# Kernel tuning notes

Measured on AMD Instinct MI355X. Metric: run time of the kernel, lower is better.

Reference implementation:

```python
import jax, jax.numpy as jnp
import numpy as np

VIEWS = 32   # hardcoded in forward
K = 5        # LocalGCN k
D = 1024     # (34-2)*(34-2) flattened conv features per view
EPS = 1e-5   # BatchNorm eps


def leaky_relu(x, slope=0.2):
    return jnp.where(x >= 0, x, slope * x)


def setup_inputs() -> dict:
    key = jax.random.key(0)
    ks = jax.random.split(key, 8)
    B_img = 512 * VIEWS
    x = jax.random.normal(ks[0], (B_img, 3, 34, 34), jnp.float32)
    vertices = jax.random.normal(ks[1], (VIEWS, 3), jnp.float32)
    # Conv2d(3, 1, 3)
    conv_w = jax.random.normal(ks[2], (1, 3, 3, 3), jnp.float32) * 0.1
    conv_b = jnp.zeros((1,), jnp.float32)
    # relation MLP R: Linear(10,10) -> ReLU -> Linear(10,1)
    r_w1 = jax.random.normal(ks[3], (10, 10), jnp.float32) * 0.3
    r_b1 = jnp.zeros((10,), jnp.float32)
    r_w2 = jax.random.normal(ks[4], (1, 10), jnp.float32) * 0.3
    r_b2 = jnp.zeros((1,), jnp.float32)
    # LocalGCN conv: Linear(D, D) + BatchNorm1d(D)
    lin_w = jax.random.normal(ks[5], (D, D), jnp.float32) / np.sqrt(D)
    lin_b = jnp.zeros((D,), jnp.float32)
    bn_g = jnp.ones((D,), jnp.float32)
    bn_b = jnp.zeros((D,), jnp.float32)
    return dict(x=x, vertices=vertices, conv_w=conv_w, conv_b=conv_b,
                r_w1=r_w1, r_b1=r_b1, r_w2=r_w2, r_b2=r_b2,
                lin_w=lin_w, lin_b=lin_b, bn_g=bn_g, bn_b=bn_b)


def reference(x, vertices, conv_w, conv_b, r_w1, r_b1, r_w2, r_b2,
              lin_w, lin_b, bn_g, bn_b):
    # Conv2d(3->1, kernel 3, valid) : (B*32,3,34,34) -> (B*32,1,32,32)
    y = jax.lax.conv_general_dilated(
        x, conv_w, window_strides=(1, 1), padding='VALID',
        dimension_numbers=('NCHW', 'OIHW', 'NCHW'))
    y = y + conv_b[None, :, None, None]

    B = x.shape[0] // VIEWS
    F = y.reshape(B, VIEWS, D)                       # (B, N, D)
    V = jnp.broadcast_to(vertices[None], (B, VIEWS, 3))  # (B, N, 3)

    # knn over vertices: negative squared pairwise distance, topk largest
    inner = -2.0 * jnp.einsum('bnd,bmd->bnm', V, V)
    xx = jnp.sum(V * V, axis=-1, keepdims=True)
    pdist = -xx - inner - jnp.swapaxes(xx, 1, 2)     # (B, N, N)
    idx = jax.lax.top_k(pdist, K)[1]                 # (B, N, K)

    # index_points gathers
    Fn = jax.vmap(lambda p, i: p[i])(F, idx)         # (B, N, K, D)
    Vn = jax.vmap(lambda p, i: p[i])(V, idx)         # (B, N, K, 3)

    v0 = jnp.broadcast_to(Vn[:, :, :1, :], Vn.shape)
    dv = v0 - Vn
    dnorm = jnp.sqrt(jnp.sum(dv * dv, axis=-1, keepdims=True) + 1e-12)
    v_F = jnp.concatenate([v0, Vn, dv, dnorm], axis=-1)   # (B, N, K, 10)

    h = jax.nn.relu(v_F @ r_w1.T + r_b1)
    e = h @ r_w2.T + r_b2                            # (B, N, K, 1)

    Fa = jnp.sum(e * Fn, axis=2)                     # (B, N, D)

    flat = Fa.reshape(-1, D)
    z = flat @ lin_w.T + lin_b
    mean = jnp.mean(z, axis=0)
    var = jnp.var(z, axis=0)
    z = (z - mean) / jnp.sqrt(var + EPS) * bn_g + bn_b
    out = leaky_relu(z).reshape(-1, 1, D)            # n_views = 1
    return out
```

## Files before the change

kernel.cpp:

```cpp
#include <hip/hip_runtime.h>
#include <stdint.h>

typedef unsigned short u16;
using bf16x8 = __attribute__((ext_vector_type(8))) short;
using f32x4  = __attribute__((ext_vector_type(4))) float;

__device__ __forceinline__ float bf2f(u16 u) {
  union { unsigned int i; float f; } a; a.i = ((unsigned int)u) << 16; return a.f;
}
__device__ __forceinline__ u16 f2bf(float f) {
  union { float f; unsigned int i; } a; a.f = f;
  unsigned int u = a.i;
  u += 0x7fffu + ((u >> 16) & 1u);
  return (u16)(u >> 16);
}
__device__ __forceinline__ float lrelu(float x) { return x >= 0.f ? x : 0.2f * x; }

__global__ __launch_bounds__(256) void prep_convw_kernel(
    const float* __restrict__ vert, const float* __restrict__ rw1,
    const float* __restrict__ rb1, const float* __restrict__ rw2,
    const float* __restrict__ rb2, const float* __restrict__ lw,
    u16* __restrict__ wb, float* __restrict__ e_out,
    int* __restrict__ idx_out, float* __restrict__ stats) {
  const int t = threadIdx.x;
  if (blockIdx.x < 1024) {
    const int i = blockIdx.x * 256 + t;
    float4 v = ((const float4*)lw)[i];
    uint2 o;
    o.x = (unsigned)f2bf(v.x) | ((unsigned)f2bf(v.y) << 16);
    o.y = (unsigned)f2bf(v.z) | ((unsigned)f2bf(v.w) << 16);
    ((uint2*)wb)[i] = o;
    return;
  }
  __shared__ float Vs[96];
  __shared__ float w1s[100];
  __shared__ float b1s[10];
  __shared__ float w2s[10];
  __shared__ float b2s;
  if (t < 96)  Vs[t]  = vert[t];
  if (t < 100) w1s[t] = rw1[t];
  if (t < 10)  { b1s[t] = rb1[t]; w2s[t] = rw2[t]; }
  if (t == 0)  b2s = rb2[0];
  for (int i = t; i < 2048; i += 256) stats[i] = 0.f;
  __syncthreads();
  if (t < 32) {
    const float vt0 = Vs[t*3], vt1 = Vs[t*3+1], vt2 = Vs[t*3+2];
    const float xxt = vt0*vt0 + vt1*vt1 + vt2*vt2;
    float pd[32];
    #pragma unroll
    for (int m = 0; m < 32; ++m) {
      float m0 = Vs[m*3], m1 = Vs[m*3+1], m2 = Vs[m*3+2];
      float dot = vt0*m0 + vt1*m1 + vt2*m2;
      float inner = -2.f * dot;
      float xxm = m0*m0 + m1*m1 + m2*m2;
      pd[m] = -xxt - inner - xxm;
    }
    int sel[5];
    unsigned taken = 0;
    #pragma unroll
    for (int k = 0; k < 5; ++k) {
      float best = -3.0e38f; int bi = 0;
      #pragma unroll
      for (int m = 0; m < 32; ++m)
        if (!((taken >> m) & 1u) && pd[m] > best) { best = pd[m]; bi = m; }
      taken |= (1u << bi);
      sel[k] = bi;
    }
    const int s0 = sel[0];
    const float v0x = Vs[s0*3], v0y = Vs[s0*3+1], v0z = Vs[s0*3+2];
    #pragma unroll
    for (int k = 0; k < 5; ++k) {
      const int si = sel[k];
      float vx = Vs[si*3], vy = Vs[si*3+1], vz = Vs[si*3+2];
      float dx = v0x - vx, dy = v0y - vy, dz = v0z - vz;
      float dn = sqrtf(dx*dx + dy*dy + dz*dz + 1e-12f);
      float vF[10] = {v0x, v0y, v0z, vx, vy, vz, dx, dy, dz, dn};
      float e = b2s;
      #pragma unroll
      for (int i = 0; i < 10; ++i) {
        float h = b1s[i];
        #pragma unroll
        for (int j = 0; j < 10; ++j) h += w1s[i*10+j] * vF[j];
        h = h > 0.f ? h : 0.f;
        e += w2s[i] * h;
      }
      e_out[t*5+k]   = e;
      idx_out[t*5+k] = sel[k];
    }
  }
}

__global__ __launch_bounds__(256) void conv_kernel(const float* __restrict__ x,
    const float* __restrict__ cw, const float* __restrict__ cb, u16* __restrict__ F) {
  __shared__ __align__(16) float lds[3*34*34];
  const int t = threadIdx.x;
  const long img = blockIdx.x;
  const float4* src = (const float4*)(x + img * 3468);
  for (int q = t; q < 867; q += 256)
    ((float4*)lds)[q] = src[q];
  float w[27];
  #pragma unroll
  for (int q = 0; q < 27; ++q) w[q] = cw[q];
  const float bias = cb[0];
  __syncthreads();
  const int p0 = t * 4;
  const int i = p0 >> 5, j = p0 & 31;
  u16 r[4];
  #pragma unroll
  for (int u = 0; u < 4; ++u) {
    float acc = bias;
    #pragma unroll
    for (int c = 0; c < 3; ++c)
      #pragma unroll
      for (int dy = 0; dy < 3; ++dy)
        #pragma unroll
        for (int dxk = 0; dxk < 3; ++dxk)
          acc += w[c*9 + dy*3 + dxk] * lds[c*1156 + (i+dy)*34 + (j+u+dxk)];
    r[u] = f2bf(acc);
  }
  uint2 o;
  o.x = (unsigned)r[0] | ((unsigned)r[1] << 16);
  o.y = (unsigned)r[2] | ((unsigned)r[3] << 16);
  ((uint2*)(F + img*1024))[t] = o;
}

__global__ __launch_bounds__(256) void gather_kernel(const u16* __restrict__ F,
    const float* __restrict__ e, const int* __restrict__ idx, u16* __restrict__ Fa) {
  const int g = blockIdx.x;
  const int b = g >> 5, n = g & 31;
  const int t = threadIdx.x;
  float a0=0.f, a1=0.f, a2=0.f, a3=0.f;
  #pragma unroll
  for (int k = 0; k < 5; ++k) {
    const float ek = e[n*5+k];
    const int id = idx[n*5+k];
    uint2 d = ((const uint2*)(F + ((long)(b*32 + id)) * 1024))[t];
    a0 += ek * __uint_as_float(d.x << 16);
    a1 += ek * __uint_as_float(d.x & 0xffff0000u);
    a2 += ek * __uint_as_float(d.y << 16);
    a3 += ek * __uint_as_float(d.y & 0xffff0000u);
  }
  uint2 o;
  o.x = (unsigned)f2bf(a0) | ((unsigned)f2bf(a1) << 16);
  o.y = (unsigned)f2bf(a2) | ((unsigned)f2bf(a3) << 16);
  ((uint2*)(Fa + (long)g * 1024))[t] = o;
}

__global__ __launch_bounds__(256) void gemm_kernel(const u16* __restrict__ A,
    const u16* __restrict__ W, const float* __restrict__ linb, u16* __restrict__ z,
    float* __restrict__ stats) {
  __shared__ __align__(16) u16 At[128*32];
  __shared__ __align__(16) u16 Bt[128*32];
  const int t = threadIdx.x;
  const int lane = t & 63;
  const int w = t >> 6;
  const int lr = lane & 15, lq = lane >> 4;
  const int wm = w >> 1, wn = w & 1;
  const long m0 = (long)blockIdx.y * 128;
  const int n0 = blockIdx.x * 128;
  f32x4 acc[4][4];
  #pragma unroll
  for (int mi = 0; mi < 4; ++mi)
    #pragma unroll
    for (int ni = 0; ni < 4; ++ni) acc[mi][ni] = (f32x4){0.f, 0.f, 0.f, 0.f};
  const int srow = t >> 2;
  const int scol = (t & 3) * 8;
  for (int k0 = 0; k0 < 1024; k0 += 32) {
    #pragma unroll
    for (int h = 0; h < 2; ++h) {
      const u16* ga = A + (m0 + h*64 + srow) * 1024 + k0 + scol;
      const u16* gb = W + (long)(n0 + h*64 + srow) * 1024 + k0 + scol;
      __builtin_amdgcn_global_load_lds(
          (const __attribute__((address_space(1))) void*)ga,
          (__attribute__((address_space(3))) void*)((char*)At + h*4096 + t*16), 16, 0, 0);
      __builtin_amdgcn_global_load_lds(
          (const __attribute__((address_space(1))) void*)gb,
          (__attribute__((address_space(3))) void*)((char*)Bt + h*4096 + t*16), 16, 0, 0);
    }
    __syncthreads();
    bf16x8 af[4], bfr[4];
    #pragma unroll
    for (int i = 0; i < 4; ++i)
      af[i] = *(const bf16x8*)&At[(wm*64 + i*16 + lr)*32 + lq*8];
    #pragma unroll
    for (int i = 0; i < 4; ++i)
      bfr[i] = *(const bf16x8*)&Bt[(wn*64 + i*16 + lr)*32 + lq*8];
    #pragma unroll
    for (int mi = 0; mi < 4; ++mi)
      #pragma unroll
      for (int ni = 0; ni < 4; ++ni)
        acc[mi][ni] = __builtin_amdgcn_mfma_f32_16x16x32_bf16(af[mi], bfr[ni], acc[mi][ni], 0, 0, 0);
    __syncthreads();
  }
  #pragma unroll
  for (int ni = 0; ni < 4; ++ni) {
    const int col = n0 + wn*64 + ni*16 + lr;
    const float bias = linb[col];
    float s = 0.f, q = 0.f;
    #pragma unroll
    for (int mi = 0; mi < 4; ++mi) {
      const long row = m0 + wm*64 + mi*16 + lq*4;
      #pragma unroll
      for (int r = 0; r < 4; ++r) {
        const float v = acc[mi][ni][r] + bias;
        z[(row + r) * 1024 + col] = f2bf(v);
        s += v; q += v * v;
      }
    }
    s += __shfl_xor(s, 16); q += __shfl_xor(q, 16);
    s += __shfl_xor(s, 32); q += __shfl_xor(q, 32);
    if (lq == 0) {
      atomicAdd(&stats[col], s);
      atomicAdd(&stats[1024 + col], q);
    }
  }
}

__global__ void finalize_kernel(float* __restrict__ stats, const float* __restrict__ g,
                                const float* __restrict__ b, int Mrows) {
  const float invM = 1.f / (float)Mrows;
  for (int c = threadIdx.x; c < 1024; c += 256) {
    float mean = stats[c] * invM;
    float var  = stats[1024+c] * invM - mean*mean;
    float rstd = rsqrtf(var + 1e-5f);
    float sc = g[c] * rstd;
    float sh = b[c] - mean * sc;
    stats[c] = sc;
    stats[1024+c] = sh;
  }
}

__global__ __launch_bounds__(256) void norm_kernel(const u16* __restrict__ z,
    const float* __restrict__ stats, float* __restrict__ out) {
  const long i = (long)blockIdx.x * 256 + threadIdx.x;
  uint2 d = ((const uint2*)z)[i];
  const int c = ((int)(i * 4)) & 1023;
  float v0 = __uint_as_float(d.x << 16);
  float v1 = __uint_as_float(d.x & 0xffff0000u);
  float v2 = __uint_as_float(d.y << 16);
  float v3 = __uint_as_float(d.y & 0xffff0000u);
  float4 y;
  y.x = lrelu(v0 * stats[c+0] + stats[1024+c+0]);
  y.y = lrelu(v1 * stats[c+1] + stats[1024+c+1]);
  y.z = lrelu(v2 * stats[c+2] + stats[1024+c+2]);
  y.w = lrelu(v3 * stats[c+3] + stats[1024+c+3]);
  ((float4*)out)[i] = y;
}

extern "C" void kernel_launch(void* const* d_in, const int* in_sizes, int n_in,
                              void* d_out, int out_size, void* d_ws, size_t ws_size,
                              hipStream_t stream) {
  const float* x    = (const float*)d_in[0];
  const float* vert = (const float*)d_in[1];
  const float* cw   = (const float*)d_in[2];
  const float* cb   = (const float*)d_in[3];
  const float* rw1  = (const float*)d_in[4];
  const float* rb1  = (const float*)d_in[5];
  const float* rw2  = (const float*)d_in[6];
  const float* rb2  = (const float*)d_in[7];
  const float* lw   = (const float*)d_in[8];
  const float* lb   = (const float*)d_in[9];
  const float* bng  = (const float*)d_in[10];
  const float* bnb  = (const float*)d_in[11];
  float* out = (float*)d_out;

  const int n_img = in_sizes[0] / (3*34*34);
  const size_t faBytes = (size_t)n_img * 1024 * 2;

  char* ws = (char*)d_ws;
  u16*  Fa = (u16*)ws;
  u16*  F  = (u16*)(ws + faBytes);
  u16*  z  = (u16*)(ws + faBytes);
  char* sp = ws + 2*faBytes;
  float* e_buf   = (float*)sp;
  int*   idx_buf = (int*)(sp + 1024);
  float* stats   = (float*)(sp + 2048);
  u16*   Wb      = (u16*)(sp + 16384);

  prep_convw_kernel<<<1025, 256, 0, stream>>>(vert, rw1, rb1, rw2, rb2, lw, Wb,
                                              e_buf, idx_buf, stats);
  conv_kernel<<<n_img, 256, 0, stream>>>(x, cw, cb, F);
  gather_kernel<<<n_img, 256, 0, stream>>>(F, e_buf, idx_buf, Fa);
  gemm_kernel<<<dim3(8, n_img/128), 256, 0, stream>>>(Fa, Wb, lb, z, stats);
  finalize_kernel<<<1, 256, 0, stream>>>(stats, bng, bnb, n_img);
  norm_kernel<<<(n_img*1024)/1024, 256, 0, stream>>>(z, stats, out);
}
```

Before: 462.1 us.

## Fuse conv with neighbor gather per batch in LDS and fold BN finalize into norm

Conv and kNN aggregation are merged into one kernel. Each block handles one batch sample: it convolves all 32 views into LDS and then gathers neighbors from LDS, so the intermediate F tensor never goes to global memory. The BN finalize kernel is removed; the normalize kernel now computes scale and shift from the raw stats inline and handles 8 elements per thread. The cost is much less parallelism: only n_img/32 blocks, each with about 78KB of LDS, looping serially over the views with barriers and no load overlap.

```diff
diff --git a/kernel.cpp b/kernel.cpp
--- a/kernel.cpp
+++ b/kernel.cpp
@@ -90,60 +90,66 @@
   }
 }
 
-__global__ __launch_bounds__(256) void conv_kernel(const float* __restrict__ x,
-    const float* __restrict__ cw, const float* __restrict__ cb, u16* __restrict__ F) {
-  __shared__ __align__(16) float lds[3*34*34];
-  const int t = threadIdx.x;
-  const long img = blockIdx.x;
-  const float4* src = (const float4*)(x + img * 3468);
-  for (int q = t; q < 867; q += 256)
-    ((float4*)lds)[q] = src[q];
+__global__ __launch_bounds__(256) void conv_gather_kernel(
+    const float* __restrict__ x, const float* __restrict__ cw,
+    const float* __restrict__ cb, const float* __restrict__ e,
+    const int* __restrict__ idx, u16* __restrict__ Fa) {
+  __shared__ __align__(16) float img[3*34*34];
+  __shared__ __align__(16) u16 Fl[32*1024];
+  __shared__ float e_s[160];
+  __shared__ int   idx_s[160];
+  const int t = threadIdx.x;
+  const long b = blockIdx.x;
+
   float w[27];
   #pragma unroll
   for (int q = 0; q < 27; ++q) w[q] = cw[q];
   const float bias = cb[0];
-  __syncthreads();
+  if (t < 160) { e_s[t] = e[t]; idx_s[t] = idx[t]; }
+
   const int p0 = t * 4;
   const int i = p0 >> 5, j = p0 & 31;
-  u16 r[4];
-  #pragma unroll
-  for (int u = 0; u < 4; ++u) {
-    float acc = bias;
-    #pragma unroll
-    for (int c = 0; c < 3; ++c)
-      #pragma unroll
-      for (int dy = 0; dy < 3; ++dy)
+  for (int v = 0; v < 32; ++v) {
+    const float4* src = (const float4*)(x + (b*32 + v) * 3468);
+    for (int q = t; q < 867; q += 256)
+      ((float4*)img)[q] = src[q];
+    __syncthreads();
+    u16 r[4];
+    #pragma unroll
+    for (int u = 0; u < 4; ++u) {
+      float acc = bias;
+      #pragma unroll
+      for (int c = 0; c < 3; ++c)
         #pragma unroll
-        for (int dxk = 0; dxk < 3; ++dxk)
-          acc += w[c*9 + dy*3 + dxk] * lds[c*1156 + (i+dy)*34 + (j+u+dxk)];
-    r[u] = f2bf(acc);
-  }
-  uint2 o;
-  o.x = (unsigned)r[0] | ((unsigned)r[1] << 16);
-  o.y = (unsigned)r[2] | ((unsigned)r[3] << 16);
-  ((uint2*)(F + img*1024))[t] = o;
-}
-
-__global__ __launch_bounds__(256) void gather_kernel(const u16* __restrict__ F,
-    const float* __restrict__ e, const int* __restrict__ idx, u16* __restrict__ Fa) {
-  const int g = blockIdx.x;
-  const int b = g >> 5, n = g & 31;
-  const int t = threadIdx.x;
-  float a0=0.f, a1=0.f, a2=0.f, a3=0.f;
-  #pragma unroll
-  for (int k = 0; k < 5; ++k) {
-    const float ek = e[n*5+k];
-    const int id = idx[n*5+k];
-    uint2 d = ((const uint2*)(F + ((long)(b*32 + id)) * 1024))[t];
-    a0 += ek * __uint_as_float(d.x << 16);
-    a1 += ek * __uint_as_float(d.x & 0xffff0000u);
-    a2 += ek * __uint_as_float(d.y << 16);
-    a3 += ek * __uint_as_float(d.y & 0xffff0000u);
-  }
-  uint2 o;
-  o.x = (unsigned)f2bf(a0) | ((unsigned)f2bf(a1) << 16);
-  o.y = (unsigned)f2bf(a2) | ((unsigned)f2bf(a3) << 16);
-  ((uint2*)(Fa + (long)g * 1024))[t] = o;
+        for (int dy = 0; dy < 3; ++dy)
+          #pragma unroll
+          for (int dxk = 0; dxk < 3; ++dxk)
+            acc += w[c*9 + dy*3 + dxk] * img[c*1156 + (i+dy)*34 + (j+u+dxk)];
+      r[u] = f2bf(acc);
+    }
+    uint2 o;
+    o.x = (unsigned)r[0] | ((unsigned)r[1] << 16);
+    o.y = (unsigned)r[2] | ((unsigned)r[3] << 16);
+    ((uint2*)(Fl + v*1024))[t] = o;
+    __syncthreads();
+  }
+  for (int n = 0; n < 32; ++n) {
+    float a0=0.f, a1=0.f, a2=0.f, a3=0.f;
+    #pragma unroll
+    for (int k = 0; k < 5; ++k) {
+      const float ek = e_s[n*5+k];
+      const int id = idx_s[n*5+k];
+      uint2 d = ((const uint2*)(Fl + id*1024))[t];
+      a0 += ek * __uint_as_float(d.x << 16);
+      a1 += ek * __uint_as_float(d.x & 0xffff0000u);
+      a2 += ek * __uint_as_float(d.y << 16);
+      a3 += ek * __uint_as_float(d.y & 0xffff0000u);
+    }
+    uint2 o;
+    o.x = (unsigned)f2bf(a0) | ((unsigned)f2bf(a1) << 16);
+    o.y = (unsigned)f2bf(a2) | ((unsigned)f2bf(a3) << 16);
+    ((uint2*)(Fa + (b*32 + n) * 1024))[t] = o;
+  }
 }
 
 __global__ __launch_bounds__(256) void gemm_kernel(const u16* __restrict__ A,
@@ -216,35 +222,32 @@
   }
 }
 
-__global__ void finalize_kernel(float* __restrict__ stats, const float* __restrict__ g,
-                                const float* __restrict__ b, int Mrows) {
-  const float invM = 1.f / (float)Mrows;
-  for (int c = threadIdx.x; c < 1024; c += 256) {
-    float mean = stats[c] * invM;
-    float var  = stats[1024+c] * invM - mean*mean;
-    float rstd = rsqrtf(var + 1e-5f);
-    float sc = g[c] * rstd;
-    float sh = b[c] - mean * sc;
-    stats[c] = sc;
-    stats[1024+c] = sh;
-  }
-}
-
 __global__ __launch_bounds__(256) void norm_kernel(const u16* __restrict__ z,
-    const float* __restrict__ stats, float* __restrict__ out) {
-  const long i = (long)blockIdx.x * 256 + threadIdx.x;
-  uint2 d = ((const uint2*)z)[i];
-  const int c = ((int)(i * 4)) & 1023;
-  float v0 = __uint_as_float(d.x << 16);
-  float v1 = __uint_as_float(d.x & 0xffff0000u);
-  float v2 = __uint_as_float(d.y << 16);
-  float v3 = __uint_as_float(d.y & 0xffff0000u);
-  float4 y;
-  y.x = lrelu(v0 * stats[c+0] + stats[1024+c+0]);
-  y.y = lrelu(v1 * stats[c+1] + stats[1024+c+1]);
-  y.z = lrelu(v2 * stats[c+2] + stats[1024+c+2]);
-  y.w = lrelu(v3 * stats[c+3] + stats[1024+c+3]);
-  ((float4*)out)[i] = y;
+    const float* __restrict__ stats, const float* __restrict__ g,
+    const float* __restrict__ bb, float invM, float* __restrict__ out) {
+  const int t = threadIdx.x;
+  const long i = (long)blockIdx.x * 256 + t;
+  uint4 d = ((const uint4*)z)[i];
+  const int c = (t & 127) * 8;
+  float vv[8];
+  vv[0] = __uint_as_float(d.x << 16); vv[1] = __uint_as_float(d.x & 0xffff0000u);
+  vv[2] = __uint_as_float(d.y << 16); vv[3] = __uint_as_float(d.y & 0xffff0000u);
+  vv[4] = __uint_as_float(d.z << 16); vv[5] = __uint_as_float(d.z & 0xffff0000u);
+  vv[6] = __uint_as_float(d.w << 16); vv[7] = __uint_as_float(d.w & 0xffff0000u);
+  float y[8];
+  #pragma unroll
+  for (int j = 0; j < 8; ++j) {
+    const int cj = c + j;
+    const float mean = stats[cj] * invM;
+    const float var  = stats[1024+cj] * invM - mean*mean;
+    const float sc = g[cj] * rsqrtf(var + 1e-5f);
+    const float sh = bb[cj] - mean * sc;
+    y[j] = lrelu(vv[j] * sc + sh);
+  }
+  float4 o0 = {y[0], y[1], y[2], y[3]};
+  float4 o1 = {y[4], y[5], y[6], y[7]};
+  ((float4*)out)[i*2]   = o0;
+  ((float4*)out)[i*2+1] = o1;
 }
 
 extern "C" void kernel_launch(void* const* d_in, const int* in_sizes, int n_in,
@@ -269,7 +272,6 @@
 
   char* ws = (char*)d_ws;
   u16*  Fa = (u16*)ws;
-  u16*  F  = (u16*)(ws + faBytes);
   u16*  z  = (u16*)(ws + faBytes);
   char* sp = ws + 2*faBytes;
   float* e_buf   = (float*)sp;
@@ -279,9 +281,7 @@
 
   prep_convw_kernel<<<1025, 256, 0, stream>>>(vert, rw1, rb1, rw2, rb2, lw, Wb,
                                               e_buf, idx_buf, stats);
-  conv_kernel<<<n_img, 256, 0, stream>>>(x, cw, cb, F);
-  gather_kernel<<<n_img, 256, 0, stream>>>(F, e_buf, idx_buf, Fa);
+  conv_gather_kernel<<<n_img/32, 256, 0, stream>>>(x, cw, cb, e_buf, idx_buf, Fa);
   gemm_kernel<<<dim3(8, n_img/128), 256, 0, stream>>>(Fa, Wb, lb, z, stats);
-  finalize_kernel<<<1, 256, 0, stream>>>(stats, bng, bnb, n_img);
-  norm_kernel<<<(n_img*1024)/1024, 256, 0, stream>>>(z, stats, out);
-}
+  norm_kernel<<<n_img/2, 256, 0, stream>>>(z, stats, bng, bnb, 1.f/(float)n_img, out);
+}
```

Result: slower. 475.3 us (+2.8%).
